# Kernel optimization log

Measured on AMD Instinct MI355X. Metric: run time of the kernel, lower is better.

The kernel has to match this reference:

```python
import jax, jax.numpy as jnp
import numpy as np

IN_FEATURES = 4096
OUT_FEATURES = 4096
ALPHA = 0.01  # dequant scale = input_scale * weight_scale
BETA = 1.0


def setup_inputs() -> dict:
    key = jax.random.key(0)
    kx, kw, kb = jax.random.split(key, 3)
    # int8 activations (W8A8): values in [-127, 127]
    x = jax.random.randint(kx, (4, 2048, IN_FEATURES), -127, 128, dtype=jnp.int8)
    # int8 weight buffer, [out_features, in_features] as in the torch module
    weight = jax.random.randint(kw, (OUT_FEATURES, IN_FEATURES), -127, 128, dtype=jnp.int8)
    # fp32 bias, [1, out_features]
    bias = jax.random.normal(kb, (1, OUT_FEATURES), dtype=jnp.float32)
    alpha = jnp.float32(ALPHA)
    return {"x": x, "weight": weight, "bias": bias, "alpha": alpha}


def reference(x, weight, bias, alpha):
    # y = alpha * (x_int8 @ W_int8^T) + beta * bias, accumulated in int32, output fp32
    x_shape = x.shape
    x2 = x.reshape(-1, x_shape[-1])  # [B*S, in]
    # int8 GEMM with int32 accumulation (faithful to the fused kernel's math)
    acc = jax.lax.dot_general(
        x2, weight,
        dimension_numbers=(((1,), (1,)), ((), ())),
        preferred_element_type=jnp.int32,
    )  # [B*S, out]
    y = alpha * acc.astype(jnp.float32) + BETA * bias  # fused dequant + bias
    return y.reshape(*x_shape[:-1], OUT_FEATURES)
```

## Files before the change

### kernel.cpp

```cpp
#include <hip/hip_runtime.h>
#include <stdint.h>

typedef int v4i __attribute__((ext_vector_type(4)));

constexpr int K_DIM = 4096;
constexpr int N_DIM = 4096;
constexpr int TM = 128;
constexpr int TN = 128;
constexpr int TK = 64;
constexpr int KSTEPS = K_DIM / TK;

__device__ __forceinline__ int pack4(int a, int b, int c, int d) {
    unsigned r = (unsigned(a) & 0xFFu)
               | ((unsigned(b) & 0xFFu) << 8)
               | ((unsigned(c) & 0xFFu) << 16)
               | (unsigned(d) << 24);
    return (int)r;
}

__global__ __launch_bounds__(256) void pack_i32_to_i8(
    const int* __restrict__ src, int8_t* __restrict__ dst, int n16)
{
    int idx = blockIdx.x * blockDim.x + threadIdx.x;
    if (idx >= n16) return;
    const v4i* s = (const v4i*)src + (size_t)idx * 4;
    v4i a = s[0], b = s[1], c = s[2], d = s[3];
    v4i o;
    o.x = pack4(a.x, a.y, a.z, a.w);
    o.y = pack4(b.x, b.y, b.z, b.w);
    o.z = pack4(c.x, c.y, c.z, c.w);
    o.w = pack4(d.x, d.y, d.z, d.w);
    ((v4i*)dst)[idx] = o;
}

__device__ __forceinline__ void gld16(const int8_t* g, int8_t* l) {
    __builtin_amdgcn_global_load_lds(
        (const __attribute__((address_space(1))) char*)g,
        (__attribute__((address_space(3))) char*)l,
        16, 0, 0);
}

__global__ __launch_bounds__(256) void w8a8_gemm_packed(
    const int8_t* __restrict__ X,
    const int8_t* __restrict__ Wt,
    const float*  __restrict__ bias,
    const float*  __restrict__ alphap,
    float* __restrict__ Y)
{
    __shared__ __align__(16) int8_t As[TM * TK];
    __shared__ __align__(16) int8_t Bs[TN * TK];

    const int tid  = threadIdx.x;
    const int lane = tid & 63;
    const int wave = tid >> 6;

    const int m0 = blockIdx.x * TM;
    const int n0 = blockIdx.y * TN;

    const int c0   = wave * 64 + lane;
    const int srow = c0 >> 2;
    const int gko  = ((c0 & 3) ^ ((srow >> 1) & 3)) << 4;

    const int8_t* Ag0 = X  + (size_t)(m0 + srow) * K_DIM + gko;
    const int8_t* Bg0 = Wt + (size_t)(n0 + srow) * K_DIM + gko;
    const size_t  half = (size_t)64 * K_DIM;

    int8_t* Al0 = As + wave * 1024;
    int8_t* Bl0 = Bs + wave * 1024;

    const int wm   = (wave & 1) << 6;
    const int wn   = (wave >> 1) << 6;
    const int lrow = lane & 15;
    const int quad = lane >> 4;

    int a_off[4], b_off[4];
#pragma unroll
    for (int i = 0; i < 4; ++i) {
        const int ra = wm + i * 16 + lrow;
        a_off[i] = ra * 64 + ((quad ^ ((ra >> 1) & 3)) << 4);
        const int rb = wn + i * 16 + lrow;
        b_off[i] = rb * 64 + ((quad ^ ((rb >> 1) & 3)) << 4);
    }

    v4i acc[4][4] = {};

    for (int kt = 0; kt < KSTEPS; ++kt) {
        const int kb = kt * TK;
        gld16(Ag0 + kb,        Al0);
        gld16(Ag0 + half + kb, Al0 + 4096);
        gld16(Bg0 + kb,        Bl0);
        gld16(Bg0 + half + kb, Bl0 + 4096);
        __syncthreads();

        v4i a[4], b[4];
#pragma unroll
        for (int i = 0; i < 4; ++i) a[i] = *(const v4i*)(As + a_off[i]);
#pragma unroll
        for (int j = 0; j < 4; ++j) b[j] = *(const v4i*)(Bs + b_off[j]);

#pragma unroll
        for (int i = 0; i < 4; ++i)
#pragma unroll
            for (int j = 0; j < 4; ++j)
                acc[i][j] = __builtin_amdgcn_mfma_i32_16x16x64_i8(a[i], b[j], acc[i][j], 0, 0, 0);

        __syncthreads();
    }

    const float alpha = *alphap;
#pragma unroll
    for (int j = 0; j < 4; ++j) {
        const int col = n0 + wn + j * 16 + lrow;
        const float bj = bias[col];
#pragma unroll
        for (int i = 0; i < 4; ++i) {
            const size_t rbase = (size_t)(m0 + wm + i * 16 + quad * 4) * N_DIM + col;
#pragma unroll
            for (int r = 0; r < 4; ++r)
                Y[rbase + (size_t)r * N_DIM] = fmaf(alpha, (float)acc[i][j][r], bj);
        }
    }
}

__global__ __launch_bounds__(256, 2) void w8a8_gemm_fb(
    const int*   __restrict__ X,
    const int*   __restrict__ Wt,
    const float* __restrict__ bias,
    const float* __restrict__ alphap,
    float* __restrict__ Y)
{
    __shared__ __align__(16) int8_t As[TM * TK];
    __shared__ __align__(16) int8_t Bs[TN * TK];

    const int tid  = threadIdx.x;
    const int lane = tid & 63;
    const int wave = tid >> 6;
    const int m0 = blockIdx.x * TM;
    const int n0 = blockIdx.y * TN;

    const int srow = tid >> 3;
    const int sk   = (tid & 7) * 8;
    const int* Ag = X  + (size_t)(m0 + srow) * K_DIM + sk;
    const int* Bg = Wt + (size_t)(n0 + srow) * K_DIM + sk;

    int wr_off[4];
#pragma unroll
    for (int r = 0; r < 4; ++r) {
        const int row = r * 32 + (tid >> 3);
        const int dw  = (tid & 7) * 2;
        const int sw  = row * 16 + (((dw >> 2) ^ ((row >> 1) & 3)) << 2) + (dw & 3);
        wr_off[r] = sw * 4;
    }

    const int wm   = (wave & 1) << 6;
    const int wn   = (wave >> 1) << 6;
    const int lrow = lane & 15;
    const int quad = lane >> 4;

    int a_off[4], b_off[4];
#pragma unroll
    for (int i = 0; i < 4; ++i) {
        const int ra = wm + i * 16 + lrow;
        a_off[i] = ra * 64 + ((quad ^ ((ra >> 1) & 3)) << 4);
        const int rb = wn + i * 16 + lrow;
        b_off[i] = rb * 64 + ((quad ^ ((rb >> 1) & 3)) << 4);
    }

    v4i acc[4][4] = {};
    v4i av[8], bv[8];
#pragma unroll
    for (int r = 0; r < 4; ++r) {
        const int* pa = Ag + (size_t)r * 32 * K_DIM;
        const int* pb = Bg + (size_t)r * 32 * K_DIM;
        av[2 * r] = *(const v4i*)(pa);  av[2 * r + 1] = *(const v4i*)(pa + 4);
        bv[2 * r] = *(const v4i*)(pb);  bv[2 * r + 1] = *(const v4i*)(pb + 4);
    }

    for (int kt = 0; kt < KSTEPS; ++kt) {
#pragma unroll
        for (int r = 0; r < 4; ++r) {
            int2 pa2, pb2;
            pa2.x = pack4(av[2*r].x,   av[2*r].y,   av[2*r].z,   av[2*r].w);
            pa2.y = pack4(av[2*r+1].x, av[2*r+1].y, av[2*r+1].z, av[2*r+1].w);
            pb2.x = pack4(bv[2*r].x,   bv[2*r].y,   bv[2*r].z,   bv[2*r].w);
            pb2.y = pack4(bv[2*r+1].x, bv[2*r+1].y, bv[2*r+1].z, bv[2*r+1].w);
            *(int2*)(As + wr_off[r]) = pa2;
            *(int2*)(Bs + wr_off[r]) = pb2;
        }
        const int kn = (kt + 1 < KSTEPS) ? (kt + 1) : kt;
        const int koff = kn * TK;
#pragma unroll
        for (int r = 0; r < 4; ++r) {
            const int* pa = Ag + (size_t)r * 32 * K_DIM + koff;
            const int* pb = Bg + (size_t)r * 32 * K_DIM + koff;
            av[2 * r] = *(const v4i*)(pa);  av[2 * r + 1] = *(const v4i*)(pa + 4);
            bv[2 * r] = *(const v4i*)(pb);  bv[2 * r + 1] = *(const v4i*)(pb + 4);
        }
        __syncthreads();
        v4i a[4], b[4];
#pragma unroll
        for (int i = 0; i < 4; ++i) a[i] = *(const v4i*)(As + a_off[i]);
#pragma unroll
        for (int j = 0; j < 4; ++j) b[j] = *(const v4i*)(Bs + b_off[j]);
#pragma unroll
        for (int i = 0; i < 4; ++i)
#pragma unroll
            for (int j = 0; j < 4; ++j)
                acc[i][j] = __builtin_amdgcn_mfma_i32_16x16x64_i8(a[i], b[j], acc[i][j], 0, 0, 0);
        __syncthreads();
    }

    const float alpha = *alphap;
#pragma unroll
    for (int j = 0; j < 4; ++j) {
        const int col = n0 + wn + j * 16 + lrow;
        const float bj = bias[col];
#pragma unroll
        for (int i = 0; i < 4; ++i) {
            const size_t rbase = (size_t)(m0 + wm + i * 16 + quad * 4) * N_DIM + col;
#pragma unroll
            for (int r = 0; r < 4; ++r)
                Y[rbase + (size_t)r * N_DIM] = fmaf(alpha, (float)acc[i][j][r], bj);
        }
    }
}

extern "C" void kernel_launch(void* const* d_in, const int* in_sizes, int n_in,
                              void* d_out, int out_size, void* d_ws, size_t ws_size,
                              hipStream_t stream) {
    const int*   X32   = (const int*)d_in[0];
    const int*   W32   = (const int*)d_in[1];
    const float* bias  = (const float*)d_in[2];
    const float* alpha = (const float*)d_in[3];
    float* Y = (float*)d_out;

    const int nX = in_sizes[0];
    const int nW = in_sizes[1];
    const int M  = nX / K_DIM;
    dim3 grid(M / TM, N_DIM / TN);

    if (ws_size >= (size_t)nX + (size_t)nW) {
        int8_t* Xp = (int8_t*)d_ws;
        int8_t* Wp = Xp + nX;
        const int nX16 = nX / 16, nW16 = nW / 16;
        pack_i32_to_i8<<<(nX16 + 255) / 256, 256, 0, stream>>>(X32, Xp, nX16);
        pack_i32_to_i8<<<(nW16 + 255) / 256, 256, 0, stream>>>(W32, Wp, nW16);
        w8a8_gemm_packed<<<grid, dim3(256), 0, stream>>>(Xp, Wp, bias, alpha, Y);
    } else {
        w8a8_gemm_fb<<<grid, dim3(256), 0, stream>>>(X32, W32, bias, alpha, Y);
    }
}
```

Measured before the change: 425.0 us.

## Double K tile to 128 in packed GEMM and fuse int8 pack kernels

```diff
diff --git a/kernel.cpp b/kernel.cpp
--- a/kernel.cpp
+++ b/kernel.cpp
@@ -7,7 +7,7 @@
 constexpr int N_DIM = 4096;
 constexpr int TM = 128;
 constexpr int TN = 128;
-constexpr int TK = 64;
+constexpr int TK = 128;
 constexpr int KSTEPS = K_DIM / TK;
 
 __device__ __forceinline__ int pack4(int a, int b, int c, int d) {
@@ -18,19 +18,18 @@
     return (int)r;
 }
 
-__global__ __launch_bounds__(256) void pack_i32_to_i8(
-    const int* __restrict__ src, int8_t* __restrict__ dst, int n16)
+__global__ __launch_bounds__(256) void pack_both(
+    const int* __restrict__ s1, int* __restrict__ d1, int n1,
+    const int* __restrict__ s2, int* __restrict__ d2, int n2)
 {
     int idx = blockIdx.x * blockDim.x + threadIdx.x;
-    if (idx >= n16) return;
-    const v4i* s = (const v4i*)src + (size_t)idx * 4;
-    v4i a = s[0], b = s[1], c = s[2], d = s[3];
-    v4i o;
-    o.x = pack4(a.x, a.y, a.z, a.w);
-    o.y = pack4(b.x, b.y, b.z, b.w);
-    o.z = pack4(c.x, c.y, c.z, c.w);
-    o.w = pack4(d.x, d.y, d.z, d.w);
-    ((v4i*)dst)[idx] = o;
+    const int* s;
+    int* d;
+    if (idx < n1) { s = s1; d = d1; }
+    else if (idx < n1 + n2) { s = s2; d = d2; idx -= n1; }
+    else return;
+    v4i v = ((const v4i*)s)[idx];
+    d[idx] = pack4(v.x, v.y, v.z, v.w);
 }
 
 __device__ __forceinline__ void gld16(const int8_t* g, int8_t* l) {
@@ -57,16 +56,18 @@
     const int m0 = blockIdx.x * TM;
     const int n0 = blockIdx.y * TN;
 
-    const int c0   = wave * 64 + lane;
-    const int srow = c0 >> 2;
-    const int gko  = ((c0 & 3) ^ ((srow >> 1) & 3)) << 4;
-
-    const int8_t* Ag0 = X  + (size_t)(m0 + srow) * K_DIM + gko;
-    const int8_t* Bg0 = Wt + (size_t)(n0 + srow) * K_DIM + gko;
-    const size_t  half = (size_t)64 * K_DIM;
-
-    int8_t* Al0 = As + wave * 1024;
-    int8_t* Bl0 = Bs + wave * 1024;
+    const int8_t* Aga[4];
+    const int8_t* Bga[4];
+    int lds_off[4];
+#pragma unroll
+    for (int i = 0; i < 4; ++i) {
+        const int c    = (wave * 4 + i) * 64 + lane;
+        const int row  = c >> 3;
+        const int gko  = ((c & 7) ^ ((row >> 1) & 7)) << 4;
+        Aga[i] = X  + (size_t)(m0 + row) * K_DIM + gko;
+        Bga[i] = Wt + (size_t)(n0 + row) * K_DIM + gko;
+        lds_off[i] = c << 4;
+    }
 
     const int wm   = (wave & 1) << 6;
     const int wn   = (wave >> 1) << 6;
@@ -77,32 +78,36 @@
 #pragma unroll
     for (int i = 0; i < 4; ++i) {
         const int ra = wm + i * 16 + lrow;
-        a_off[i] = ra * 64 + ((quad ^ ((ra >> 1) & 3)) << 4);
+        a_off[i] = ra * TK + ((quad ^ ((ra >> 1) & 7)) << 4);
         const int rb = wn + i * 16 + lrow;
-        b_off[i] = rb * 64 + ((quad ^ ((rb >> 1) & 3)) << 4);
+        b_off[i] = rb * TK + ((quad ^ ((rb >> 1) & 7)) << 4);
     }
 
     v4i acc[4][4] = {};
 
     for (int kt = 0; kt < KSTEPS; ++kt) {
         const int kb = kt * TK;
-        gld16(Ag0 + kb,        Al0);
-        gld16(Ag0 + half + kb, Al0 + 4096);
-        gld16(Bg0 + kb,        Bl0);
-        gld16(Bg0 + half + kb, Bl0 + 4096);
-        __syncthreads();
-
-        v4i a[4], b[4];
-#pragma unroll
-        for (int i = 0; i < 4; ++i) a[i] = *(const v4i*)(As + a_off[i]);
-#pragma unroll
-        for (int j = 0; j < 4; ++j) b[j] = *(const v4i*)(Bs + b_off[j]);
-
-#pragma unroll
-        for (int i = 0; i < 4; ++i)
-#pragma unroll
-            for (int j = 0; j < 4; ++j)
-                acc[i][j] = __builtin_amdgcn_mfma_i32_16x16x64_i8(a[i], b[j], acc[i][j], 0, 0, 0);
+#pragma unroll
+        for (int i = 0; i < 4; ++i) {
+            gld16(Aga[i] + kb, As + lds_off[i]);
+            gld16(Bga[i] + kb, Bs + lds_off[i]);
+        }
+        __syncthreads();
+
+#pragma unroll
+        for (int kk = 0; kk < 2; ++kk) {
+            const int kx = kk << 6;
+            v4i a[4], b[4];
+#pragma unroll
+            for (int i = 0; i < 4; ++i) a[i] = *(const v4i*)(As + (a_off[i] ^ kx));
+#pragma unroll
+            for (int j = 0; j < 4; ++j) b[j] = *(const v4i*)(Bs + (b_off[j] ^ kx));
+#pragma unroll
+            for (int i = 0; i < 4; ++i)
+#pragma unroll
+                for (int j = 0; j < 4; ++j)
+                    acc[i][j] = __builtin_amdgcn_mfma_i32_16x16x64_i8(a[i], b[j], acc[i][j], 0, 0, 0);
+        }
 
         __syncthreads();
     }
@@ -129,8 +134,8 @@
     const float* __restrict__ alphap,
     float* __restrict__ Y)
 {
-    __shared__ __align__(16) int8_t As[TM * TK];
-    __shared__ __align__(16) int8_t Bs[TN * TK];
+    __shared__ __align__(16) int8_t As[TM * 64];
+    __shared__ __align__(16) int8_t Bs[TN * 64];
 
     const int tid  = threadIdx.x;
     const int lane = tid & 63;
@@ -176,7 +181,7 @@
         bv[2 * r] = *(const v4i*)(pb);  bv[2 * r + 1] = *(const v4i*)(pb + 4);
     }
 
-    for (int kt = 0; kt < KSTEPS; ++kt) {
+    for (int kt = 0; kt < 64; ++kt) {
 #pragma unroll
         for (int r = 0; r < 4; ++r) {
             int2 pa2, pb2;
@@ -187,8 +192,8 @@
             *(int2*)(As + wr_off[r]) = pa2;
             *(int2*)(Bs + wr_off[r]) = pb2;
         }
-        const int kn = (kt + 1 < KSTEPS) ? (kt + 1) : kt;
-        const int koff = kn * TK;
+        const int kn = (kt + 1 < 64) ? (kt + 1) : kt;
+        const int koff = kn * 64;
 #pragma unroll
         for (int r = 0; r < 4; ++r) {
             const int* pa = Ag + (size_t)r * 32 * K_DIM + koff;
@@ -242,9 +247,10 @@
     if (ws_size >= (size_t)nX + (size_t)nW) {
         int8_t* Xp = (int8_t*)d_ws;
         int8_t* Wp = Xp + nX;
-        const int nX16 = nX / 16, nW16 = nW / 16;
-        pack_i32_to_i8<<<(nX16 + 255) / 256, 256, 0, stream>>>(X32, Xp, nX16);
-        pack_i32_to_i8<<<(nW16 + 255) / 256, 256, 0, stream>>>(W32, Wp, nW16);
+        const int n1 = nX / 4, n2 = nW / 4;
+        const int nthreads = n1 + n2;
+        pack_both<<<(nthreads + 255) / 256, 256, 0, stream>>>(
+            X32, (int*)Xp, n1, W32, (int*)Wp, n2);
         w8a8_gemm_packed<<<grid, dim3(256), 0, stream>>>(Xp, Wp, bias, alpha, Y);
     } else {
         w8a8_gemm_fb<<<grid, dim3(256), 0, stream>>>(X32, W32, bias, alpha, Y);
```

Result: no change. 420.1 us (-1.1%).
